# Performance work log

Measured on AMD Instinct MI355X. Metric: run time of the kernel, lower is better.

Reference implementation:

```python
import jax, jax.numpy as jnp
import numpy as np

MAX_SHIFT = 4.0  # init max_shift; stored shifts are pre-divided by it
Q = 3            # Maclaurin order


def setup_inputs() -> dict:
    key = jax.random.key(0)
    k1, k2, k3, k4 = jax.random.split(key, 4)
    x = jax.random.normal(k1, (16, 64, 112, 112), jnp.float32)
    # weights: (out_channels, q*in_channels, k, k)
    weights = jax.random.normal(k2, (128, 192, 3, 3), jnp.float32) * 0.05
    bias = jax.random.normal(k3, (128,), jnp.float32) * 0.05
    # stored shifts buffer: uniform(-max_shift, max_shift) then /= max_shift -> [-1, 1]
    shifts = jax.random.uniform(k4, (64, 2), jnp.float32, -1.0, 1.0)
    return {"x": x, "weights": weights, "bias": bias, "shifts": shifts}


def _shift_one_channel(xc, sx, sy):
    """Bilinear translate one channel by (sx, sy) pixels, zero padding.
    Equivalent to F.affine_grid(identity + [sx/(W/2), sy/(H/2)]) + grid_sample
    (align_corners=False): out[n, i, j] = x[n, i + sy, j + sx] (bilinear).
    xc: (N, H, W)."""
    N, H, W = xc.shape
    jx = jnp.arange(W, dtype=xc.dtype) + sx  # sampled x coord per output col
    iy = jnp.arange(H, dtype=xc.dtype) + sy  # sampled y coord per output row
    x0f = jnp.floor(jx)
    y0f = jnp.floor(iy)
    wx = jx - x0f  # (W,)
    wy = iy - y0f  # (H,)
    x0 = x0f.astype(jnp.int32)
    y0 = y0f.astype(jnp.int32)

    def gather(yi, xi):
        vy = (yi >= 0) & (yi < H)
        vx = (xi >= 0) & (xi < W)
        yc = jnp.clip(yi, 0, H - 1)
        xcl = jnp.clip(xi, 0, W - 1)
        v = xc[:, yc, :][:, :, xcl]  # (N, H, W)
        return v * (vy[:, None] & vx[None, :]).astype(xc.dtype)

    return ((1 - wy)[:, None] * (1 - wx)[None, :] * gather(y0, x0)
            + (1 - wy)[:, None] * wx[None, :] * gather(y0, x0 + 1)
            + wy[:, None] * (1 - wx)[None, :] * gather(y0 + 1, x0)
            + wy[:, None] * wx[None, :] * gather(y0 + 1, x0 + 1))


def reference(x, weights, bias, shifts):
    s = shifts * MAX_SHIFT  # pixel shifts, (C_in, 2) = (sx, sy)
    # per-channel bilinear shift (vmap over channel axis)
    shifted = jax.vmap(_shift_one_channel, in_axes=(1, 0, 0), out_axes=1)(
        x, s[:, 0], s[:, 1])  # (N, C, H, W)
    # Maclaurin powers concatenated along channels: (N, q*C, H, W)
    y = jnp.concatenate([shifted ** i for i in range(1, Q + 1)], axis=1)
    out = jax.lax.conv_general_dilated(
        y, weights, window_strides=(1, 1), padding=[(1, 1), (1, 1)],
        dimension_numbers=("NCHW", "OIHW", "NCHW"))
    return out + bias[None, :, None, None]
```

## Files before the change

kernel.cpp:

```cpp
#include <hip/hip_runtime.h>
#include <hip/hip_bf16.h>

typedef __bf16 bf16x8 __attribute__((ext_vector_type(8)));
typedef float  f32x4  __attribute__((ext_vector_type(4)));

#define H_DIM 112
#define W_DIM 112
#define CIN 64
#define CMID 192
#define COUT 128
#define NB 16

__device__ __forceinline__ void dma16(const void* g, void* l) {
    __builtin_amdgcn_global_load_lds(
        (const __attribute__((address_space(1))) unsigned*)g,
        (__attribute__((address_space(3))) unsigned*)l, 16, 0, 0);
}

__global__ __launch_bounds__(256) void repack_w_kernel(
    const float* __restrict__ w, __hip_bfloat16* __restrict__ wr)
{
    int idx = blockIdx.x * 256 + threadIdx.x;
    if (idx < 9 * COUT * CMID) {
        int ci  = idx % CMID;
        int t   = idx / CMID;
        int co  = t % COUT;
        int khw = t / COUT;
        wr[idx] = __float2bfloat16(w[(co * CMID + ci) * 9 + khw]);
    }
}

__global__ __launch_bounds__(256) void shift_pow_kernel(
    const float* __restrict__ x, const float* __restrict__ shifts,
    __hip_bfloat16* __restrict__ y)
{
    __shared__ __align__(16) float xs[64 * 116];
    __shared__ __align__(16) __hip_bfloat16 tile[112 * 104];
    __shared__ float4 prm[32];

    const int tid = threadIdx.x;
    const int h   = blockIdx.x;
    const int cb  = blockIdx.y * 32;
    const int n   = blockIdx.z;

    if (tid < 32) {
        float sx = shifts[2 * (cb + tid)]     * 4.0f;
        float sy = shifts[2 * (cb + tid) + 1] * 4.0f;
        float fx = floorf(sx), fy = floorf(sy);
        prm[tid] = make_float4(fx, fy, sx - fx, sy - fy);
    }
    __syncthreads();

    #pragma unroll
    for (int k = 0; k < 7; ++k) {
        int i     = k * 256 + tid;
        int rowid = i / 28;
        int part  = i - rowid * 28;
        int c = rowid >> 1, t = rowid & 1;
        int iy = (int)prm[c].y;
        int r  = h + iy + t;
        bool valid = (unsigned)r < (unsigned)H_DIM;
        int rr = min(max(r, 0), H_DIM - 1);
        float4 v = ((const float4*)(
            x + ((size_t)(n * CIN + cb + c) * H_DIM + rr) * W_DIM))[part];
        if (!valid) v = make_float4(0.f, 0.f, 0.f, 0.f);
        *(float4*)&xs[rowid * 116 + part * 4] = v;
    }
    __syncthreads();

    #pragma unroll
    for (int k = 0; k < 14; ++k) {
        int i  = k * 256 + tid;
        int c  = i / 112;
        int px = i - c * 112;
        float4 p = prm[c];
        int ix = (int)p.x;
        float wx = p.z, wy = p.w;
        int q0 = px + ix, q1 = q0 + 1;
        float f0 = ((unsigned)q0 < (unsigned)W_DIM) ? 1.f : 0.f;
        float f1 = ((unsigned)q1 < (unsigned)W_DIM) ? 1.f : 0.f;
        int a0 = min(max(q0, 0), W_DIM - 1);
        int a1 = min(max(q1, 0), W_DIM - 1);
        const float* r0 = &xs[(2 * c) * 116];
        const float* r1 = &xs[(2 * c + 1) * 116];
        float top = (1.f - wx) * f0 * r0[a0] + wx * f1 * r0[a1];
        float bot = (1.f - wx) * f0 * r1[a0] + wx * f1 * r1[a1];
        float v  = (1.f - wy) * top + wy * bot;
        float v2 = v * v, v3 = v2 * v;
        __hip_bfloat16* tp = &tile[px * 104];
        tp[c]      = __float2bfloat16(v);
        tp[c + 32] = __float2bfloat16(v2);
        tp[c + 64] = __float2bfloat16(v3);
    }
    __syncthreads();

    const float4* tl4 = (const float4*)tile;
    float4* yo4 = (float4*)(y + ((size_t)(n * H_DIM + h) * W_DIM) * CMID);
    const int cbd4 = cb >> 3;
    #pragma unroll
    for (int k = 0; k < 6; ++k) {
        int i = k * 256 + tid;
        if (i < 1344) {
            int px  = i / 12;
            int cp4 = i - px * 12;
            int chunk = cp4 >> 2, e4 = cp4 & 3;
            yo4[px * 24 + chunk * 8 + cbd4 + e4] = tl4[px * 13 + cp4];
        }
    }
}

#define YSTR_E 104
#define BUF_E  12288

#define CONV_GROUP(G, CUR, NXT) do {                                          \
    const int c3_ = (G) / 3, kw_ = (G) % 3;                                   \
    if ((G) < 8) {                                                            \
        const int c3n_ = ((G) + 1) / 3, kwn_ = ((G) + 1) % 3;                 \
        _Pragma("unroll")                                                     \
        for (int nt = 0; nt < 7; ++nt)                                        \
            NXT[nt] = *(const bf16x8*)(lbase +                                \
                (nt * 16 + kwn_) * YSTR_E + c3n_ * 32);                       \
    }                                                                         \
    _Pragma("unroll")                                                         \
    for (int nt = 0; nt < 7; ++nt) {                                          \
        acc[0][nt] = __builtin_amdgcn_mfma_f32_16x16x32_bf16(                 \
            af[c3_][kw_][0], CUR[nt], acc[0][nt], 0, 0, 0);                   \
        acc[1][nt] = __builtin_amdgcn_mfma_f32_16x16x32_bf16(                 \
            af[c3_][kw_][1], CUR[nt], acc[1][nt], 0, 0, 0);                   \
    }                                                                         \
    if ((G) < 8) {                                                            \
        _Pragma("unroll")                                                     \
        for (int k_ = 0; k_ < 7; ++k_) {                                      \
            __builtin_amdgcn_sched_group_barrier(0x100, 1, 0);   \
            __builtin_amdgcn_sched_group_barrier(0x008, 2, 0);    \
        }                                                                     \
    } else {                                                                  \
        __builtin_amdgcn_sched_group_barrier(0x008, 14, 0);                   \
    }                                                                         \
} while (0)

__global__ __launch_bounds__(256, 2) void conv_kernel(
    const __bf16* __restrict__ y,
    const __bf16* __restrict__ wr,
    const float* __restrict__ bias,
    float* __restrict__ out)
{
    __shared__ __align__(16) __bf16 ybuf[2][BUF_E];

    const int tid  = threadIdx.x;
    const int lane = tid & 63;
    const int wid  = tid >> 6;
    const int m    = lane & 15;
    const int quad = lane >> 4;

    const int bid = blockIdx.x;
    const int id  = (bid & 7) * 224 + (bid >> 3);
    const int n   = id / H_DIM;
    const int h   = id - n * H_DIM;

    if (tid < 208) {
        int b    = tid >= 104;
        int r    = tid - b * 104;
        int slot = (r >= 52) ? 113 : 0;
        int dw   = (r >= 52) ? r - 52 : r;
        ((unsigned*)&ybuf[b][0])[slot * 52 + dw] = 0u;
    }

    int dj[6];
    #pragma unroll
    for (int j = 0; j < 6; ++j) {
        int t = 4 * j + wid;
        int o = 208 + 1024 * t + 16 * lane;
        int slot = o / 208;
        int rem  = o - slot * 208;
        dj[j] = (t < 23 && rem < 192 && slot <= 112)
                    ? ((slot - 1) * 384 + rem) : -1;
    }

    f32x4 acc[2][7];
    #pragma unroll
    for (int mt = 0; mt < 2; ++mt)
        #pragma unroll
        for (int nt = 0; nt < 7; ++nt)
            #pragma unroll
            for (int r = 0; r < 4; ++r) acc[mt][nt][r] = 0.0f;

    const char* ybase = (const char*)y + (size_t)n * (H_DIM * W_DIM * CMID * 2);

    const int f = (h == 0)         ? 2 : 0;
    const int l = (h == H_DIM - 1) ? 3 : 5;

    {
        int row = h + (f >> 1) - 1, half = f & 1;
        const char* src = ybase + (size_t)row * (W_DIM * CMID * 2) + half * 192;
        char* lb = (char*)&ybuf[0][0];
        #pragma unroll
        for (int j = 0; j < 6; ++j) {
            int t = 4 * j + wid;
            if (dj[j] >= 0) dma16(src + dj[j], lb + 208 + 1024 * t);
        }
    }
    __syncthreads();

    int buf = 0;
    for (int s = f; s <= l; ++s) {
        const int kh = s >> 1, half = s & 1;

        bf16x8 af[3][3][2];
        #pragma unroll
        for (int c3 = 0; c3 < 3; ++c3)
            #pragma unroll
            for (int kw = 0; kw < 3; ++kw)
                #pragma unroll
                for (int mt = 0; mt < 2; ++mt)
                    af[c3][kw][mt] = *(const bf16x8*)(
                        wr + (size_t)((kh * 3 + kw) * COUT + wid * 32 + mt * 16 + m) * CMID
                           + half * 96 + c3 * 32 + quad * 8);

        __builtin_amdgcn_sched_barrier(0);

        if (s < l) {
            int row = h + ((s + 1) >> 1) - 1, halfn = (s + 1) & 1;
            const char* src = ybase + (size_t)row * (W_DIM * CMID * 2) + halfn * 192;
            char* lb = (char*)&ybuf[buf ^ 1][0];
            #pragma unroll
            for (int j = 0; j < 6; ++j) {
                int t = 4 * j + wid;
                if (dj[j] >= 0) dma16(src + dj[j], lb + 208 + 1024 * t);
            }
        }

        const __bf16* lbase = &ybuf[buf][m * YSTR_E + quad * 8];

        bf16x8 bA[7], bB[7];
        #pragma unroll
        for (int nt = 0; nt < 7; ++nt)
            bA[nt] = *(const bf16x8*)(lbase + (nt * 16 + 0) * YSTR_E + 0 * 32);
        __builtin_amdgcn_sched_group_barrier(0x100, 7, 0);

        CONV_GROUP(0, bA, bB);
        CONV_GROUP(1, bB, bA);
        CONV_GROUP(2, bA, bB);
        CONV_GROUP(3, bB, bA);
        CONV_GROUP(4, bA, bB);
        CONV_GROUP(5, bB, bA);
        CONV_GROUP(6, bA, bB);
        CONV_GROUP(7, bB, bA);
        CONV_GROUP(8, bA, bB);

        __syncthreads();
        buf ^= 1;
    }

    #pragma unroll
    for (int mt = 0; mt < 2; ++mt) {
        const int co0 = wid * 32 + mt * 16 + quad * 4;
        float bv[4];
        #pragma unroll
        for (int rr = 0; rr < 4; ++rr) bv[rr] = bias[co0 + rr];
        #pragma unroll
        for (int nt = 0; nt < 7; ++nt) {
            int j = nt * 16 + m;
            #pragma unroll
            for (int rr = 0; rr < 4; ++rr) {
                out[(((size_t)n * COUT + co0 + rr) * H_DIM + h) * W_DIM + j] =
                    acc[mt][nt][rr] + bv[rr];
            }
        }
    }
}

extern "C" void kernel_launch(void* const* d_in, const int* in_sizes, int n_in,
                              void* d_out, int out_size, void* d_ws, size_t ws_size,
                              hipStream_t stream) {
    const float* x      = (const float*)d_in[0];
    const float* w      = (const float*)d_in[1];
    const float* bias   = (const float*)d_in[2];
    const float* shifts = (const float*)d_in[3];
    float* out = (float*)d_out;

    __hip_bfloat16* y  = (__hip_bfloat16*)d_ws;
    __hip_bfloat16* wr = (__hip_bfloat16*)((char*)d_ws + 77070336);

    repack_w_kernel<<<dim3((9 * COUT * CMID + 255) / 256), 256, 0, stream>>>(w, wr);
    shift_pow_kernel<<<dim3(H_DIM, 2, NB), 256, 0, stream>>>(x, shifts, y);
    conv_kernel<<<dim3(H_DIM * NB), 256, 0, stream>>>(
        (const __bf16*)y, (const __bf16*)wr, bias, out);
}
```

Baseline: 274.0 us.

## Derive kw-shifted B fragments via DPP row shifts instead of LDS reloads

Loads only the center (kw=1) B fragment from LDS per channel chunk and builds the kw=0 and kw=2 fragments with DPP row_shr/row_shl lane shuffles. Only edge lanes (m==0 or m==15) reload from LDS. A runtime probe picks which DPP control gives the needed direction. This targets LDS read bandwidth in the conv inner loop, at the cost of many extra VALU DPP ops and selects per MFMA group, plus divergent edge loads.

```diff
diff --git a/kernel.cpp b/kernel.cpp
--- a/kernel.cpp
+++ b/kernel.cpp
@@ -112,27 +112,71 @@
 #define YSTR_E 104
 #define BUF_E  12288
 
-#define CONV_GROUP(G, CUR, NXT) do {                                          \
-    const int c3_ = (G) / 3, kw_ = (G) % 3;                                   \
-    if ((G) < 8) {                                                            \
-        const int c3n_ = ((G) + 1) / 3, kwn_ = ((G) + 1) % 3;                 \
-        _Pragma("unroll")                                                     \
-        for (int nt = 0; nt < 7; ++nt)                                        \
-            NXT[nt] = *(const bf16x8*)(lbase +                                \
-                (nt * 16 + kwn_) * YSTR_E + c3n_ * 32);                       \
-    }                                                                         \
+__device__ __forceinline__ bf16x8 dpp_sel(bf16x8 v, bool pick101) {
+    union { bf16x8 f; int i[4]; } a, r;
+    a.f = v;
+    #pragma unroll
+    for (int d = 0; d < 4; ++d) {
+        int x = __builtin_amdgcn_update_dpp(a.i[d], a.i[d], 0x101, 0xF, 0xF, false);
+        int y = __builtin_amdgcn_update_dpp(a.i[d], a.i[d], 0x111, 0xF, 0xF, false);
+        r.i[d] = pick101 ? x : y;
+    }
+    return r.f;
+}
+
+#define CONV_C3(C3, BF1, BF1N, READ_NEXT) do {                                \
+    bf16x8 e0[7], e2[7];                                                      \
+          \
     _Pragma("unroll")                                                         \
     for (int nt = 0; nt < 7; ++nt) {                                          \
+        e0[nt] = dpp_sel(BF1[nt], dn101);                                     \
+        if (m == 0)                                                           \
+            e0[nt] = *(const bf16x8*)(lbase + (nt * 16) * YSTR_E + (C3) * 32);\
         acc[0][nt] = __builtin_amdgcn_mfma_f32_16x16x32_bf16(                 \
-            af[c3_][kw_][0], CUR[nt], acc[0][nt], 0, 0, 0);                   \
+            af[C3][1][0], BF1[nt], acc[0][nt], 0, 0, 0);                      \
         acc[1][nt] = __builtin_amdgcn_mfma_f32_16x16x32_bf16(                 \
-            af[c3_][kw_][1], CUR[nt], acc[1][nt], 0, 0, 0);                   \
-    }                                                                         \
-    if ((G) < 8) {                                                            \
+            af[C3][1][1], BF1[nt], acc[1][nt], 0, 0, 0);                      \
+    }                                                                         \
+    _Pragma("unroll")                                                         \
+    for (int k_ = 0; k_ < 7; ++k_) {                                          \
+        __builtin_amdgcn_sched_group_barrier(0x002, 12, 0);        \
+        __builtin_amdgcn_sched_group_barrier(0x100, 1, 0);         \
+        __builtin_amdgcn_sched_group_barrier(0x008, 2, 0);         \
+    }                                                                         \
+           \
+    _Pragma("unroll")                                                         \
+    for (int nt = 0; nt < 7; ++nt) {                                          \
+        e2[nt] = dpp_sel(BF1[nt], up101);                                     \
+        if (m == 15)                                                          \
+            e2[nt] = *(const bf16x8*)(lbase +                                 \
+                (nt * 16 + 2) * YSTR_E + (C3) * 32);                          \
+        acc[0][nt] = __builtin_amdgcn_mfma_f32_16x16x32_bf16(                 \
+            af[C3][0][0], e0[nt], acc[0][nt], 0, 0, 0);                       \
+        acc[1][nt] = __builtin_amdgcn_mfma_f32_16x16x32_bf16(                 \
+            af[C3][0][1], e0[nt], acc[1][nt], 0, 0, 0);                       \
+    }                                                                         \
+    _Pragma("unroll")                                                         \
+    for (int k_ = 0; k_ < 7; ++k_) {                                          \
+        __builtin_amdgcn_sched_group_barrier(0x002, 12, 0);                   \
+        __builtin_amdgcn_sched_group_barrier(0x100, 1, 0);                    \
+        __builtin_amdgcn_sched_group_barrier(0x008, 2, 0);                    \
+    }                                                                         \
+                    \
+    _Pragma("unroll")                                                         \
+    for (int nt = 0; nt < 7; ++nt) {                                          \
+        if (READ_NEXT)                                                        \
+            BF1N[nt] = *(const bf16x8*)(lbase +                               \
+                (nt * 16 + 1) * YSTR_E + ((C3) + 1) * 32);                    \
+        acc[0][nt] = __builtin_amdgcn_mfma_f32_16x16x32_bf16(                 \
+            af[C3][2][0], e2[nt], acc[0][nt], 0, 0, 0);                       \
+        acc[1][nt] = __builtin_amdgcn_mfma_f32_16x16x32_bf16(                 \
+            af[C3][2][1], e2[nt], acc[1][nt], 0, 0, 0);                       \
+    }                                                                         \
+    if (READ_NEXT) {                                                          \
         _Pragma("unroll")                                                     \
         for (int k_ = 0; k_ < 7; ++k_) {                                      \
-            __builtin_amdgcn_sched_group_barrier(0x100, 1, 0);   \
-            __builtin_amdgcn_sched_group_barrier(0x008, 2, 0);    \
+            __builtin_amdgcn_sched_group_barrier(0x100, 1, 0);                \
+            __builtin_amdgcn_sched_group_barrier(0x008, 2, 0);                \
         }                                                                     \
     } else {                                                                  \
         __builtin_amdgcn_sched_group_barrier(0x008, 14, 0);                   \
@@ -152,6 +196,10 @@
     const int wid  = tid >> 6;
     const int m    = lane & 15;
     const int quad = lane >> 4;
+
+    const int probe = __builtin_amdgcn_update_dpp(0, (int)lane, 0x101, 0xF, 0xF, true);
+    const bool up101 = (__builtin_amdgcn_readfirstlane(probe) == 1);
+    const bool dn101 = !up101;
 
     const int bid = blockIdx.x;
     const int id  = (bid & 7) * 224 + (bid >> 3);
@@ -232,21 +280,15 @@
 
         const __bf16* lbase = &ybuf[buf][m * YSTR_E + quad * 8];
 
-        bf16x8 bA[7], bB[7];
+        bf16x8 bC[7], bD[7];
         #pragma unroll
         for (int nt = 0; nt < 7; ++nt)
-            bA[nt] = *(const bf16x8*)(lbase + (nt * 16 + 0) * YSTR_E + 0 * 32);
+            bC[nt] = *(const bf16x8*)(lbase + (nt * 16 + 1) * YSTR_E + 0 * 32);
         __builtin_amdgcn_sched_group_barrier(0x100, 7, 0);
 
-        CONV_GROUP(0, bA, bB);
-        CONV_GROUP(1, bB, bA);
-        CONV_GROUP(2, bA, bB);
-        CONV_GROUP(3, bB, bA);
-        CONV_GROUP(4, bA, bB);
-        CONV_GROUP(5, bB, bA);
-        CONV_GROUP(6, bA, bB);
-        CONV_GROUP(7, bB, bA);
-        CONV_GROUP(8, bA, bB);
+        CONV_C3(0, bC, bD, 1);
+        CONV_C3(1, bD, bC, 1);
+        CONV_C3(2, bC, bD, 0);
 
         __syncthreads();
         buf ^= 1;
```

After: 293.1 us. 1.07x slower.
